# Performance work log

Hardware: AMD Instinct MI355X
Metric: run time of the kernel (lower is better)

The kernel has to match this reference:

```python
import jax, jax.numpy as jnp
import numpy as np
from jax import lax

# BatchNorm2d(affine=False) in eval mode with initial running stats (mean=0, var=1)
# reduces to a constant scale. (Original torch module in train mode would use batch
# stats of the dispatched subset; we use the eval-mode form for a deterministic,
# vectorizable reference.)
BN_SCALE = 1.0 / np.sqrt(1.0 + 1e-5)
DN = ('NCHW', 'OIHW', 'NCHW')


def _dw(x, w, pad, dil=1):
    # depthwise conv, kernel [C,1,k,k]
    return lax.conv_general_dilated(x, w, (1, 1), [(pad, pad), (pad, pad)],
                                    rhs_dilation=(dil, dil), dimension_numbers=DN,
                                    feature_group_count=x.shape[1])


def _pw(x, w):
    # pointwise 1x1 conv, kernel [C,C,1,1]
    return lax.conv_general_dilated(x, w, (1, 1), 'VALID', dimension_numbers=DN)


def _sep(x, d1, p1, d2, p2, pad):
    # DARTS SepConv: (ReLU-dw-pw-BN) x 2
    y = _pw(_dw(jax.nn.relu(x), d1, pad), p1) * BN_SCALE
    return _pw(_dw(jax.nn.relu(y), d2, pad), p2) * BN_SCALE


def _dil(x, d, p, pad):
    # DARTS DilConv: ReLU-dw(dilation=2)-pw-BN
    return _pw(_dw(jax.nn.relu(x), d, pad, 2), p) * BN_SCALE


def _maxpool3(x):
    y = jnp.pad(x, ((0, 0), (0, 0), (1, 1), (1, 1)), constant_values=-jnp.inf)
    return lax.reduce_window(y, -jnp.inf, lax.max, (1, 1, 3, 3), (1, 1, 1, 1), 'VALID')


def _avgpool3(x):
    # avg_pool 3x3 stride 1 pad 1, count_include_pad=False
    pad = [(0, 0), (0, 0), (1, 1), (1, 1)]
    s = lax.reduce_window(x, 0.0, lax.add, (1, 1, 3, 3), (1, 1, 1, 1), pad)
    c = lax.reduce_window(jnp.ones_like(x), 0.0, lax.add, (1, 1, 3, 3), (1, 1, 1, 1), pad)
    return s / c


def _mixed_forward(x, weights, params, top):
    B, n_op = weights.shape
    _, idx = lax.top_k(weights, top)                    # [B, top]
    sel = jax.nn.one_hot(idx, n_op).sum(axis=1) > 0     # [B, n_op] bool: op in top-k
    # softmax over logits masked to -inf outside top-k => non-selected ops weight 0
    gate = jax.nn.softmax(jnp.where(sel, weights, -jnp.inf), axis=-1)  # [B, n_op]
    (sc3_d1, sc3_p1, sc3_d2, sc3_p2,
     sc5_d1, sc5_p1, sc5_d2, sc5_p2,
     dc3_d, dc3_p, dc5_d, dc5_p) = params
    # PRIMITIVES order: none, max_pool_3x3, avg_pool_3x3, skip_connect,
    # sep_conv_3x3, sep_conv_5x5, dil_conv_3x3, dil_conv_5x5
    op_outs = [
        None,                        # 'none' contributes zeros
        _maxpool3(x) * BN_SCALE,     # pool ops are followed by BN(affine=False)
        _avgpool3(x) * BN_SCALE,
        x,                           # skip_connect (stride=1 -> Identity)
        _sep(x, sc3_d1, sc3_p1, sc3_d2, sc3_p2, 1),
        _sep(x, sc5_d1, sc5_p1, sc5_d2, sc5_p2, 2),
        _dil(x, dc3_d, dc3_p, 2),
        _dil(x, dc5_d, dc5_p, 4),
    ]
    out = jnp.zeros_like(x)
    for i, y in enumerate(op_outs):
        if y is not None:
            out = out + gate[:, i, None, None, None] * y
    return out, weights  # second output is gate_value_cp (clone of gate input)


def setup_inputs():
    key = jax.random.key(0)
    ks = jax.random.split(key, 16)
    B, C, H, W = 64, 128, 32, 32
    def p(k, shape):
        return jax.random.normal(k, shape, jnp.float32) * 0.05
    return {
        'x': jax.random.normal(ks[0], (B, C, H, W), jnp.float32),
        'weights': jax.random.normal(ks[1], (B, 8), jnp.float32),
        'sc3_d1': p(ks[2], (C, 1, 3, 3)), 'sc3_p1': p(ks[3], (C, C, 1, 1)),
        'sc3_d2': p(ks[4], (C, 1, 3, 3)), 'sc3_p2': p(ks[5], (C, C, 1, 1)),
        'sc5_d1': p(ks[6], (C, 1, 5, 5)), 'sc5_p1': p(ks[7], (C, C, 1, 1)),
        'sc5_d2': p(ks[8], (C, 1, 5, 5)), 'sc5_p2': p(ks[9], (C, C, 1, 1)),
        'dc3_d': p(ks[10], (C, 1, 3, 3)), 'dc3_p': p(ks[11], (C, C, 1, 1)),
        'dc5_d': p(ks[12], (C, 1, 5, 5)), 'dc5_p': p(ks[13], (C, C, 1, 1)),
        'top': 2,
    }


def reference(x, weights, sc3_d1, sc3_p1, sc3_d2, sc3_p2, sc5_d1, sc5_p1, sc5_d2, sc5_p2, dc3_d, dc3_p, dc5_d, dc5_p, top):
    params = (sc3_d1, sc3_p1, sc3_d2, sc3_p2, sc5_d1, sc5_p1, sc5_d2, sc5_p2,
              dc3_d, dc3_p, dc5_d, dc5_p)
    return _mixed_forward(x, weights, params, top)
```

## Files before the change

kernel.cpp:

```cpp
#include <hip/hip_runtime.h>
#include <hip/hip_bf16.h>


#define BN_SCALE 0.9999950000374997f
#define BB 64
#define CC 128
#define HH 32
#define WW 32
#define PLANE (HH*WW)
#define SAMP (CC*PLANE)
#define NOUT0 (BB*SAMP)

__device__ __forceinline__ float us2f(unsigned int u) {
    unsigned int x = (u & 0xffffu) << 16;
    float f; __builtin_memcpy(&f, &x, 4); return f;
}
__device__ __forceinline__ unsigned short f2us(float f) {
    __hip_bfloat16 h = __float2bfloat16(f);
    unsigned short u; __builtin_memcpy(&u, &h, 2); return u;
}

__global__ void k_gates(const float* __restrict__ wlog,
                        const void* __restrict__ topp,
                        float* __restrict__ gates,
                        int* __restrict__ cnum, int* __restrict__ cops,
                        float* __restrict__ out_w) {
    int b = threadIdx.x;

    int top = -1;
    {
        unsigned int u0 = *(const unsigned int*)topp;
        int i32 = (int)u0;
        if (i32 >= 1 && i32 <= 8) top = i32;
        else {
            float f32; __builtin_memcpy(&f32, &u0, 4);
            if (f32 >= 1.f && f32 <= 8.f) top = (int)(f32 + 0.5f);
            else { float fb = us2f(u0); if (fb >= 1.f && fb <= 8.f) top = (int)(fb + 0.5f); }
        }
        if (top < 1 || top > 8) top = 2;
    }

    float lw[8];
    #pragma unroll
    for (int i = 0; i < 8; ++i) {
        lw[i] = wlog[b * 8 + i];
        out_w[b * 8 + i] = lw[i];
    }
    bool sel[8] = {false,false,false,false,false,false,false,false};
    for (int t = 0; t < top; ++t) {
        int best = -1; float bv = -3.4e38f;
        #pragma unroll
        for (int i = 0; i < 8; ++i)
            if (!sel[i] && lw[i] > bv) { bv = lw[i]; best = i; }
        if (best >= 0) sel[best] = true;
    }
    float m = -3.4e38f;
    #pragma unroll
    for (int i = 0; i < 8; ++i) if (sel[i] && lw[i] > m) m = lw[i];
    float s = 0.f, e[8];
    #pragma unroll
    for (int i = 0; i < 8; ++i) { e[i] = sel[i] ? expf(lw[i] - m) : 0.f; s += e[i]; }
    float inv = (s > 0.f) ? 1.f / s : 0.f;
    float g[8];
    #pragma unroll
    for (int i = 0; i < 8; ++i) {
        g[i] = (s > 0.f) ? e[i] * inv : (sel[i] ? 1.f / (float)top : 0.f);
        gates[b * 8 + i] = g[i];
    }
    int n = 0;
    #pragma unroll
    for (int i = 4; i < 8; ++i)
        if (g[i] > 0.f) { cops[b * 2 + (n < 2 ? n : 1)] = i; ++n; }
    cnum[b] = (n < 2) ? n : 2;
}

template <int K, int DIL>
__device__ __forceinline__ void dw_comp(const float* __restrict__ sx,
                                        const float* __restrict__ wd, int c,
                                        unsigned short* __restrict__ opp) {
    constexpr int PAD = (K / 2) * DIL;
    float wk[K * K];
    #pragma unroll
    for (int i = 0; i < K * K; ++i) wk[i] = wd[c * K * K + i];
    #pragma unroll
    for (int j = 0; j < 4; ++j) {
        int px = threadIdx.x + j * 256;
        int h = px >> 5, w = px & 31;
        float acc = 0.f;
        #pragma unroll
        for (int ky = 0; ky < K; ++ky) {
            int ih = h + ky * DIL - PAD;
            if ((unsigned)ih >= HH) continue;
            #pragma unroll
            for (int kx = 0; kx < K; ++kx) {
                int iw = w + kx * DIL - PAD;
                if ((unsigned)iw >= WW) continue;
                acc = fmaf(wk[ky * K + kx], sx[ih * WW + iw], acc);
            }
        }
        opp[px] = f2us(acc);
    }
}

__global__ __launch_bounds__(256) void
k_dw_first(const float* __restrict__ x,
           const float* __restrict__ w4, const float* __restrict__ w5,
           const float* __restrict__ w6, const float* __restrict__ w7,
           const float* __restrict__ gates,
           unsigned short* __restrict__ A4, unsigned short* __restrict__ A5,
           unsigned short* __restrict__ P6, unsigned short* __restrict__ P7) {
    int plane = blockIdx.x;
    int b = plane >> 7, c = plane & 127;
    float g4 = gates[b * 8 + 4], g5 = gates[b * 8 + 5];
    float g6 = gates[b * 8 + 6], g7 = gates[b * 8 + 7];
    if (g4 == 0.f && g5 == 0.f && g6 == 0.f && g7 == 0.f) return;
    __shared__ float sx[PLANE];
    {
        float4 v = ((const float4*)(x + (size_t)plane * PLANE))[threadIdx.x];
        ((float4*)sx)[threadIdx.x] =
            make_float4(fmaxf(v.x, 0.f), fmaxf(v.y, 0.f),
                        fmaxf(v.z, 0.f), fmaxf(v.w, 0.f));
    }
    __syncthreads();
    size_t off = (size_t)plane * PLANE;
    if (g4 != 0.f) dw_comp<3, 1>(sx, w4, c, A4 + off);
    if (g5 != 0.f) dw_comp<5, 1>(sx, w5, c, A5 + off);
    if (g6 != 0.f) dw_comp<3, 2>(sx, w6, c, P6 + off);
    if (g7 != 0.f) dw_comp<5, 2>(sx, w7, c, P7 + off);
}

__global__ __launch_bounds__(256) void
k_dw_second(const unsigned short* __restrict__ B4,
            const unsigned short* __restrict__ B5,
            const float* __restrict__ w4, const float* __restrict__ w5,
            const float* __restrict__ gates,
            unsigned short* __restrict__ P4, unsigned short* __restrict__ P5) {
    int plane = blockIdx.x;
    int b = plane >> 7, c = plane & 127;
    float g4 = gates[b * 8 + 4], g5 = gates[b * 8 + 5];
    if (g4 == 0.f && g5 == 0.f) return;
    __shared__ float sx[PLANE];
    size_t off = (size_t)plane * PLANE;
    if (g4 != 0.f) {
        ushort4 v = ((const ushort4*)(B4 + off))[threadIdx.x];
        ((float4*)sx)[threadIdx.x] =
            make_float4(fmaxf(us2f(v.x), 0.f), fmaxf(us2f(v.y), 0.f),
                        fmaxf(us2f(v.z), 0.f), fmaxf(us2f(v.w), 0.f));
        __syncthreads();
        dw_comp<3, 1>(sx, w4, c, P4 + off);
        __syncthreads();
    }
    if (g5 != 0.f) {
        ushort4 v = ((const ushort4*)(B5 + off))[threadIdx.x];
        ((float4*)sx)[threadIdx.x] =
            make_float4(fmaxf(us2f(v.x), 0.f), fmaxf(us2f(v.y), 0.f),
                        fmaxf(us2f(v.z), 0.f), fmaxf(us2f(v.w), 0.f));
        __syncthreads();
        dw_comp<5, 1>(sx, w5, c, P5 + off);
    }
}

__device__ __forceinline__ void pw_acc(const unsigned short* __restrict__ ib,
                                       const float* __restrict__ W,
                                       int co0, int hw, float2* acc) {
    for (int ci = 0; ci < CC; ++ci) {
        unsigned int raw = *reinterpret_cast<const unsigned int*>(ib + ci * PLANE + hw);
        float vx = us2f(raw), vy = us2f(raw >> 16);
        #pragma unroll
        for (int k = 0; k < 8; ++k) {
            float wv = W[(co0 + k) * CC + ci];
            acc[k].x = fmaf(wv, vx, acc[k].x);
            acc[k].y = fmaf(wv, vy, acc[k].y);
        }
    }
}

__global__ __launch_bounds__(256) void
k_pw_mid(const unsigned short* __restrict__ A4,
         const unsigned short* __restrict__ A5,
         const float* __restrict__ W4, const float* __restrict__ W5,
         const float* __restrict__ gates,
         unsigned short* __restrict__ B4, unsigned short* __restrict__ B5) {
    int blk = blockIdx.x;
    int hws = blk & 1;
    int cog = (blk >> 1) & 15;
    int b   = (blk >> 5) & 63;
    int opi = blk >> 11;
    float g = gates[b * 8 + 4 + opi];
    if (g == 0.f) return;
    const unsigned short* in = (opi ? A5 : A4) + (size_t)b * SAMP;
    const float* W = opi ? W5 : W4;
    unsigned short* ob = (opi ? B5 : B4);
    int co0 = cog * 8;
    int hw = hws * 512 + threadIdx.x * 2;
    float2 acc[8];
    #pragma unroll
    for (int k = 0; k < 8; ++k) acc[k] = make_float2(0.f, 0.f);
    pw_acc(in, W, co0, hw, acc);
    #pragma unroll
    for (int k = 0; k < 8; ++k) {
        size_t idx = (size_t)(b * CC + co0 + k) * PLANE + hw;
        unsigned int* p = reinterpret_cast<unsigned int*>(ob + idx);
        *p = (unsigned int)f2us(BN_SCALE * acc[k].x) |
             ((unsigned int)f2us(BN_SCALE * acc[k].y) << 16);
    }
}

__global__ __launch_bounds__(256) void
k_pw_final(const float* __restrict__ x,
           const unsigned short* __restrict__ P4,
           const unsigned short* __restrict__ P5,
           const unsigned short* __restrict__ P6,
           const unsigned short* __restrict__ P7,
           const float* __restrict__ W4, const float* __restrict__ W5,
           const float* __restrict__ W6, const float* __restrict__ W7,
           const float* __restrict__ gates,
           const int* __restrict__ cnum, const int* __restrict__ cops,
           float* __restrict__ out) {
    int blk = blockIdx.x;
    int hws = blk & 1;
    int cog = (blk >> 1) & 15;
    int b = blk >> 5;
    int co0 = cog * 8;
    int hw = hws * 512 + threadIdx.x * 2;

    float g1 = gates[b * 8 + 1] * BN_SCALE;
    float g2 = gates[b * 8 + 2] * BN_SCALE;
    float g3 = gates[b * 8 + 3];
    bool haspool = (g1 != 0.f) | (g2 != 0.f) | (g3 != 0.f);

    __shared__ float sxp[8 * 18 * 32];
    int r0 = hws * 16;
    if (haspool) {
        for (int li = threadIdx.x; li < 8 * 18 * 8; li += 256) {
            int ch = li / 144, rem = li - ch * 144;
            int row = rem >> 3, c4 = rem & 7;
            int gr = r0 + row - 1;
            if ((unsigned)gr < HH) {
                float4 v = *(const float4*)(x + ((size_t)(b * CC + co0 + ch) * HH + gr) * WW + c4 * 4);
                *(float4*)(sxp + (ch * 18 + row) * 32 + c4 * 4) = v;
            }
        }
        __syncthreads();
    }

    float2 acc[8];
    #pragma unroll
    for (int k = 0; k < 8; ++k) acc[k] = make_float2(0.f, 0.f);
    int n = cnum[b];
    for (int t = 0; t < n; ++t) {
        int op = cops[b * 2 + t];
        float gs = gates[b * 8 + op] * BN_SCALE;
        const unsigned short* src;
        const float* W;
        switch (op) {
            case 4:  src = P4; W = W4; break;
            case 5:  src = P5; W = W5; break;
            case 6:  src = P6; W = W6; break;
            default: src = P7; W = W7; break;
        }
        float2 a2[8];
        #pragma unroll
        for (int k = 0; k < 8; ++k) a2[k] = make_float2(0.f, 0.f);
        pw_acc(src + (size_t)b * SAMP, W, co0, hw, a2);
        #pragma unroll
        for (int k = 0; k < 8; ++k) {
            acc[k].x = fmaf(gs, a2[k].x, acc[k].x);
            acc[k].y = fmaf(gs, a2[k].y, acc[k].y);
        }
    }

    int h = hw >> 5, w = hw & 31;
    int lr = h - r0 + 1;
    #pragma unroll
    for (int k = 0; k < 8; ++k) {
        float2 o = acc[k];
        if (haspool) {
            const float* sp = sxp + k * 18 * 32;
            #pragma unroll
            for (int jj = 0; jj < 2; ++jj) {
                int ww = w + jj;
                float mx = -3.4e38f, sm = 0.f;
                int cnt = 0;
                #pragma unroll
                for (int dh = -1; dh <= 1; ++dh) {
                    int ih = h + dh;
                    if ((unsigned)ih >= HH) continue;
                    #pragma unroll
                    for (int dw = -1; dw <= 1; ++dw) {
                        int iw = ww + dw;
                        if ((unsigned)iw >= WW) continue;
                        float v = sp[(lr + dh) * 32 + iw];
                        mx = fmaxf(mx, v);
                        sm += v;
                        ++cnt;
                    }
                }
                float pv = g1 * mx + g2 * (sm / (float)cnt) + g3 * sp[lr * 32 + ww];
                if (jj == 0) o.x += pv; else o.y += pv;
            }
        }
        *(float2*)(out + (size_t)(b * CC + co0 + k) * PLANE + hw) = o;
    }
}

extern "C" void kernel_launch(void* const* d_in, const int* in_sizes, int n_in,
                              void* d_out, int out_size, void* d_ws, size_t ws_size,
                              hipStream_t stream) {
    const float* x      = (const float*)d_in[0];
    const float* wlog   = (const float*)d_in[1];
    const float* sc3_d1 = (const float*)d_in[2];
    const float* sc3_p1 = (const float*)d_in[3];
    const float* sc3_d2 = (const float*)d_in[4];
    const float* sc3_p2 = (const float*)d_in[5];
    const float* sc5_d1 = (const float*)d_in[6];
    const float* sc5_p1 = (const float*)d_in[7];
    const float* sc5_d2 = (const float*)d_in[8];
    const float* sc5_p2 = (const float*)d_in[9];
    const float* dc3_d  = (const float*)d_in[10];
    const float* dc3_p  = (const float*)d_in[11];
    const float* dc5_d  = (const float*)d_in[12];
    const float* dc5_p  = (const float*)d_in[13];
    const void* topp    = d_in[14];

    float* out  = (float*)d_out;
    float* outw = out + NOUT0;

    float* gates = (float*)d_ws;
    int*   cnum  = (int*)((char*)d_ws + 2048);
    int*   cops  = (int*)((char*)d_ws + 2304);
    unsigned short* base = (unsigned short*)((char*)d_ws + 4096);
    unsigned short* A4 = base;
    unsigned short* A5 = base + (size_t)NOUT0;
    unsigned short* B4 = base + (size_t)NOUT0 * 2;
    unsigned short* B5 = base + (size_t)NOUT0 * 3;
    unsigned short* P4 = base + (size_t)NOUT0 * 4;
    unsigned short* P5 = base + (size_t)NOUT0 * 5;
    unsigned short* P6 = base + (size_t)NOUT0 * 6;
    unsigned short* P7 = base + (size_t)NOUT0 * 7;

    k_gates<<<1, 64, 0, stream>>>(wlog, topp, gates, cnum, cops, outw);
    k_dw_first<<<BB * CC, 256, 0, stream>>>(x, sc3_d1, sc5_d1, dc3_d, dc5_d,
                                            gates, A4, A5, P6, P7);
    k_pw_mid<<<2 * BB * 32, 256, 0, stream>>>(A4, A5, sc3_p1, sc5_p1, gates, B4, B5);
    k_dw_second<<<BB * CC, 256, 0, stream>>>(B4, B5, sc3_d2, sc5_d2, gates, P4, P5);
    k_pw_final<<<BB * 32, 256, 0, stream>>>(x, P4, P5, P6, P7,
                                            sc3_p2, sc5_p2, dc3_p, dc5_p,
                                            gates, cnum, cops, out);
}
```

Baseline: 209.4 us.

## Stage pointwise weights in LDS and widen per-thread register tiles

The pointwise conv kernels now stage a 16-output-channel weight slice in shared memory, padded to avoid bank conflicts and pre-scaled by BN scale or gate. Each thread computes 8 channels by 4 pixels instead of 8 by 2, halving the grid and doubling reuse of each activation load. The pool input tile is stored in shared memory as bf16, which halves LDS use but rounds the pool inputs. The cops buffer grows to 4 entries per sample, and the extra block syncs add overhead for each selected op.

```diff
diff --git a/kernel.cpp b/kernel.cpp
--- a/kernel.cpp
+++ b/kernel.cpp
@@ -70,8 +70,8 @@
     int n = 0;
     #pragma unroll
     for (int i = 4; i < 8; ++i)
-        if (g[i] > 0.f) { cops[b * 2 + (n < 2 ? n : 1)] = i; ++n; }
-    cnum[b] = (n < 2) ? n : 2;
+        if (g[i] > 0.f) { if (n < 4) cops[b * 4 + n] = i; ++n; }
+    cnum[b] = (n < 4) ? n : 4;
 }
 
 template <int K, int DIL>
@@ -160,17 +160,35 @@
     }
 }
 
-__device__ __forceinline__ void pw_acc(const unsigned short* __restrict__ ib,
-                                       const float* __restrict__ W,
-                                       int co0, int hw, float2* acc) {
+#define WLROW 17
+
+__device__ __forceinline__ void stage_w(float* __restrict__ Wl,
+                                        const float* __restrict__ W,
+                                        int co0, float s) {
+    #pragma unroll
+    for (int i = 0; i < 8; ++i) {
+        int idx = threadIdx.x + i * 256;
+        int c = idx >> 7, ci = idx & 127;
+        Wl[ci * WLROW + c] = W[(co0 + c) * CC + ci] * s;
+    }
+}
+
+__device__ __forceinline__ void pw_fat(const unsigned short* __restrict__ ib,
+                                       const float* __restrict__ Wl,
+                                       int cg, int hw, float acc[8][4]) {
+    const float* wr0 = Wl + cg * 8;
     for (int ci = 0; ci < CC; ++ci) {
-        unsigned int raw = *reinterpret_cast<const unsigned int*>(ib + ci * PLANE + hw);
-        float vx = us2f(raw), vy = us2f(raw >> 16);
+        uint2 raw = *reinterpret_cast<const uint2*>(ib + ci * PLANE + hw);
+        float v0 = us2f(raw.x), v1 = us2f(raw.x >> 16);
+        float v2 = us2f(raw.y), v3 = us2f(raw.y >> 16);
+        const float* wr = wr0 + ci * WLROW;
         #pragma unroll
         for (int k = 0; k < 8; ++k) {
-            float wv = W[(co0 + k) * CC + ci];
-            acc[k].x = fmaf(wv, vx, acc[k].x);
-            acc[k].y = fmaf(wv, vy, acc[k].y);
+            float wv = wr[k];
+            acc[k][0] = fmaf(wv, v0, acc[k][0]);
+            acc[k][1] = fmaf(wv, v1, acc[k][1]);
+            acc[k][2] = fmaf(wv, v2, acc[k][2]);
+            acc[k][3] = fmaf(wv, v3, acc[k][3]);
         }
     }
 }
@@ -182,27 +200,28 @@
          const float* __restrict__ gates,
          unsigned short* __restrict__ B4, unsigned short* __restrict__ B5) {
     int blk = blockIdx.x;
-    int hws = blk & 1;
-    int cog = (blk >> 1) & 15;
-    int b   = (blk >> 5) & 63;
-    int opi = blk >> 11;
-    float g = gates[b * 8 + 4 + opi];
-    if (g == 0.f) return;
-    const unsigned short* in = (opi ? A5 : A4) + (size_t)b * SAMP;
-    const float* W = opi ? W5 : W4;
-    unsigned short* ob = (opi ? B5 : B4);
-    int co0 = cog * 8;
-    int hw = hws * 512 + threadIdx.x * 2;
-    float2 acc[8];
-    #pragma unroll
-    for (int k = 0; k < 8; ++k) acc[k] = make_float2(0.f, 0.f);
-    pw_acc(in, W, co0, hw, acc);
+    int tile = blk & 15;
+    int opi  = (blk >> 4) & 1;
+    int b    = blk >> 5;
+    if (gates[b * 8 + 4 + opi] == 0.f) return;
+    int cog = tile >> 1, hws = tile & 1;
+    int co0 = cog * 16;
+    int cg = threadIdx.x >> 7, ht = threadIdx.x & 127;
+    int hw = hws * 512 + ht * 4;
+    __shared__ float Wl[128 * WLROW];
+    stage_w(Wl, opi ? W5 : W4, co0, BN_SCALE);
+    __syncthreads();
+    const unsigned short* ib = (opi ? A5 : A4) + (size_t)b * SAMP;
+    float acc[8][4] = {};
+    pw_fat(ib, Wl, cg, hw, acc);
+    unsigned short* ob = opi ? B5 : B4;
     #pragma unroll
     for (int k = 0; k < 8; ++k) {
-        size_t idx = (size_t)(b * CC + co0 + k) * PLANE + hw;
-        unsigned int* p = reinterpret_cast<unsigned int*>(ob + idx);
-        *p = (unsigned int)f2us(BN_SCALE * acc[k].x) |
-             ((unsigned int)f2us(BN_SCALE * acc[k].y) << 16);
+        size_t idx = (size_t)(b * CC + co0 + cg * 8 + k) * PLANE + hw;
+        uint2 pk;
+        pk.x = (unsigned int)f2us(acc[k][0]) | ((unsigned int)f2us(acc[k][1]) << 16);
+        pk.y = (unsigned int)f2us(acc[k][2]) | ((unsigned int)f2us(acc[k][3]) << 16);
+        *reinterpret_cast<uint2*>(ob + idx) = pk;
     }
 }
 
@@ -218,38 +237,41 @@
            const int* __restrict__ cnum, const int* __restrict__ cops,
            float* __restrict__ out) {
     int blk = blockIdx.x;
-    int hws = blk & 1;
-    int cog = (blk >> 1) & 15;
-    int b = blk >> 5;
-    int co0 = cog * 8;
-    int hw = hws * 512 + threadIdx.x * 2;
+    int tile = blk & 15;
+    int b    = blk >> 4;
+    int cog = tile >> 1, hws = tile & 1;
+    int co0 = cog * 16;
+    int cg = threadIdx.x >> 7, ht = threadIdx.x & 127;
+    int hw = hws * 512 + ht * 4;
 
     float g1 = gates[b * 8 + 1] * BN_SCALE;
     float g2 = gates[b * 8 + 2] * BN_SCALE;
     float g3 = gates[b * 8 + 3];
     bool haspool = (g1 != 0.f) | (g2 != 0.f) | (g3 != 0.f);
 
-    __shared__ float sxp[8 * 18 * 32];
+    __shared__ float Wl[128 * WLROW];
+    __shared__ unsigned short sxp[16 * 18 * 32];
+
     int r0 = hws * 16;
     if (haspool) {
-        for (int li = threadIdx.x; li < 8 * 18 * 8; li += 256) {
+        for (int li = threadIdx.x; li < 16 * 18 * 8; li += 256) {
             int ch = li / 144, rem = li - ch * 144;
             int row = rem >> 3, c4 = rem & 7;
             int gr = r0 + row - 1;
             if ((unsigned)gr < HH) {
                 float4 v = *(const float4*)(x + ((size_t)(b * CC + co0 + ch) * HH + gr) * WW + c4 * 4);
-                *(float4*)(sxp + (ch * 18 + row) * 32 + c4 * 4) = v;
+                ushort4 pv;
+                pv.x = f2us(v.x); pv.y = f2us(v.y); pv.z = f2us(v.z); pv.w = f2us(v.w);
+                *(ushort4*)(sxp + (ch * 18 + row) * 32 + c4 * 4) = pv;
             }
         }
-        __syncthreads();
-    }
-
-    float2 acc[8];
-    #pragma unroll
-    for (int k = 0; k < 8; ++k) acc[k] = make_float2(0.f, 0.f);
+    }
+    __syncthreads();
+
+    float acc[8][4] = {};
     int n = cnum[b];
     for (int t = 0; t < n; ++t) {
-        int op = cops[b * 2 + t];
+        int op = cops[b * 4 + t];
         float gs = gates[b * 8 + op] * BN_SCALE;
         const unsigned short* src;
         const float* W;
@@ -259,26 +281,20 @@
             case 6:  src = P6; W = W6; break;
             default: src = P7; W = W7; break;
         }
-        float2 a2[8];
-        #pragma unroll
-        for (int k = 0; k < 8; ++k) a2[k] = make_float2(0.f, 0.f);
-        pw_acc(src + (size_t)b * SAMP, W, co0, hw, a2);
-        #pragma unroll
-        for (int k = 0; k < 8; ++k) {
-            acc[k].x = fmaf(gs, a2[k].x, acc[k].x);
-            acc[k].y = fmaf(gs, a2[k].y, acc[k].y);
-        }
+        __syncthreads();
+        stage_w(Wl, W, co0, gs);
+        __syncthreads();
+        pw_fat(src + (size_t)b * SAMP, Wl, cg, hw, acc);
     }
 
     int h = hw >> 5, w = hw & 31;
     int lr = h - r0 + 1;
     #pragma unroll
     for (int k = 0; k < 8; ++k) {
-        float2 o = acc[k];
         if (haspool) {
-            const float* sp = sxp + k * 18 * 32;
+            const unsigned short* sp = sxp + (cg * 8 + k) * 18 * 32;
             #pragma unroll
-            for (int jj = 0; jj < 2; ++jj) {
+            for (int jj = 0; jj < 4; ++jj) {
                 int ww = w + jj;
                 float mx = -3.4e38f, sm = 0.f;
                 int cnt = 0;
@@ -290,17 +306,18 @@
                     for (int dw = -1; dw <= 1; ++dw) {
                         int iw = ww + dw;
                         if ((unsigned)iw >= WW) continue;
-                        float v = sp[(lr + dh) * 32 + iw];
+                        float v = us2f(sp[(lr + dh) * 32 + iw]);
                         mx = fmaxf(mx, v);
                         sm += v;
                         ++cnt;
                     }
                 }
-                float pv = g1 * mx + g2 * (sm / (float)cnt) + g3 * sp[lr * 32 + ww];
-                if (jj == 0) o.x += pv; else o.y += pv;
+                acc[k][jj] += g1 * mx + g2 * (sm / (float)cnt)
+                            + g3 * us2f(sp[lr * 32 + ww]);
             }
         }
-        *(float2*)(out + (size_t)(b * CC + co0 + k) * PLANE + hw) = o;
+        *(float4*)(out + (size_t)(b * CC + co0 + cg * 8 + k) * PLANE + hw) =
+            make_float4(acc[k][0], acc[k][1], acc[k][2], acc[k][3]);
     }
 }
 
@@ -342,9 +359,9 @@
     k_gates<<<1, 64, 0, stream>>>(wlog, topp, gates, cnum, cops, outw);
     k_dw_first<<<BB * CC, 256, 0, stream>>>(x, sc3_d1, sc5_d1, dc3_d, dc5_d,
                                             gates, A4, A5, P6, P7);
-    k_pw_mid<<<2 * BB * 32, 256, 0, stream>>>(A4, A5, sc3_p1, sc5_p1, gates, B4, B5);
+    k_pw_mid<<<BB * 32, 256, 0, stream>>>(A4, A5, sc3_p1, sc5_p1, gates, B4, B5);
     k_dw_second<<<BB * CC, 256, 0, stream>>>(B4, B5, sc3_d2, sc5_d2, gates, P4, P5);
-    k_pw_final<<<BB * 32, 256, 0, stream>>>(x, P4, P5, P6, P7,
+    k_pw_final<<<BB * 16, 256, 0, stream>>>(x, P4, P5, P6, P7,
                                             sc3_p2, sc5_p2, dc3_p, dc5_p,
                                             gates, cnum, cops, out);
 }
```

New measurement: 214.2 us. +2.3%, slower.

## Use bf16 MFMA for pointwise convs and split pooling into separate kernel

Applied to the files above, without the earlier changes.

Replaces the scalar FMA pointwise 1x1 convolutions in the mid and final stages with LDS-staged bf16 MFMA 16x16x32 tiles. Each block computes 64 output channels by 64 pixels, with weights converted to bf16 and the gate scale folded in. Pooling and skip terms move to a new per-plane kernel that writes the output first, and the final pointwise kernel then accumulates into it with a read-modify-write. The weights are now rounded to bf16, which adds precision error, and the extra pass plus output reread adds memory traffic.

```diff
diff --git a/kernel.cpp b/kernel.cpp
--- a/kernel.cpp
+++ b/kernel.cpp
@@ -10,6 +10,10 @@
 #define PLANE (HH*WW)
 #define SAMP (CC*PLANE)
 #define NOUT0 (BB*SAMP)
+#define LROW 136
+
+typedef __attribute__((ext_vector_type(8))) short bf16x8;
+typedef __attribute__((ext_vector_type(4))) float f32x4;
 
 __device__ __forceinline__ float us2f(unsigned int u) {
     unsigned int x = (u & 0xffffu) << 16;
@@ -70,8 +74,49 @@
     int n = 0;
     #pragma unroll
     for (int i = 4; i < 8; ++i)
-        if (g[i] > 0.f) { cops[b * 2 + (n < 2 ? n : 1)] = i; ++n; }
-    cnum[b] = (n < 2) ? n : 2;
+        if (g[i] > 0.f) { if (n < 4) cops[b * 4 + n] = i; ++n; }
+    cnum[b] = (n < 4) ? n : 4;
+}
+
+__global__ __launch_bounds__(256) void
+k_pools(const float* __restrict__ x,
+        const float* __restrict__ gates,
+        float* __restrict__ out) {
+    int plane = blockIdx.x;
+    int b = plane >> 7;
+    float g1 = gates[b * 8 + 1] * BN_SCALE;
+    float g2 = gates[b * 8 + 2] * BN_SCALE;
+    float g3 = gates[b * 8 + 3];
+    float* op = out + (size_t)plane * PLANE;
+    if (g1 == 0.f && g2 == 0.f && g3 == 0.f) {
+        ((float4*)op)[threadIdx.x] = make_float4(0.f, 0.f, 0.f, 0.f);
+        return;
+    }
+    __shared__ float sx[PLANE];
+    ((float4*)sx)[threadIdx.x] = ((const float4*)(x + (size_t)plane * PLANE))[threadIdx.x];
+    __syncthreads();
+    #pragma unroll
+    for (int j = 0; j < 4; ++j) {
+        int px = threadIdx.x + j * 256;
+        int h = px >> 5, w = px & 31;
+        float mx = -3.4e38f, sm = 0.f;
+        int cnt = 0;
+        #pragma unroll
+        for (int dh = -1; dh <= 1; ++dh) {
+            int ih = h + dh;
+            if ((unsigned)ih >= HH) continue;
+            #pragma unroll
+            for (int dw = -1; dw <= 1; ++dw) {
+                int iw = w + dw;
+                if ((unsigned)iw >= WW) continue;
+                float v = sx[ih * WW + iw];
+                mx = fmaxf(mx, v);
+                sm += v;
+                ++cnt;
+            }
+        }
+        op[px] = g1 * mx + g2 * (sm / (float)cnt) + g3 * sx[px];
+    }
 }
 
 template <int K, int DIL>
@@ -160,17 +205,46 @@
     }
 }
 
-__device__ __forceinline__ void pw_acc(const unsigned short* __restrict__ ib,
-                                       const float* __restrict__ W,
-                                       int co0, int hw, float2* acc) {
-    for (int ci = 0; ci < CC; ++ci) {
-        unsigned int raw = *reinterpret_cast<const unsigned int*>(ib + ci * PLANE + hw);
-        float vx = us2f(raw), vy = us2f(raw >> 16);
-        #pragma unroll
-        for (int k = 0; k < 8; ++k) {
-            float wv = W[(co0 + k) * CC + ci];
-            acc[k].x = fmaf(wv, vx, acc[k].x);
-            acc[k].y = fmaf(wv, vy, acc[k].y);
+
+__device__ __forceinline__ void stage_wt(unsigned short* __restrict__ Wt,
+                                         const float* __restrict__ W,
+                                         int co0, float s) {
+    unsigned int* Wtu = (unsigned int*)Wt;
+    #pragma unroll
+    for (int i = 0; i < 16; ++i) {
+        int idx = threadIdx.x + i * 256;
+        int r = idx >> 6, c2 = idx & 63;
+        float2 v = *(const float2*)(W + (size_t)(co0 + r) * CC + c2 * 2);
+        Wtu[r * (LROW / 2) + c2] =
+            (unsigned int)f2us(v.x * s) | ((unsigned int)f2us(v.y * s) << 16);
+    }
+}
+
+__device__ __forceinline__ void stage_bt(unsigned short* __restrict__ Bt,
+                                         const unsigned short* __restrict__ ib,
+                                         int hw0) {
+    #pragma unroll
+    for (int i = 0; i < 16; ++i) {
+        int idx = threadIdx.x + i * 256;
+        int ci = idx >> 5, hp = (idx & 31) * 2;
+        unsigned int raw = *(const unsigned int*)(ib + (size_t)ci * PLANE + hw0 + hp);
+        Bt[hp * LROW + ci]       = (unsigned short)(raw & 0xffffu);
+        Bt[(hp + 1) * LROW + ci] = (unsigned short)(raw >> 16);
+    }
+}
+
+__device__ __forceinline__ void mfma_tile(const unsigned short* __restrict__ Wt,
+                                          const unsigned short* __restrict__ Bt,
+                                          int wave, int quad, int m,
+                                          f32x4 acc[4]) {
+    #pragma unroll
+    for (int kb = 0; kb < 4; ++kb) {
+        int cio = kb * 32 + quad * 8;
+        bf16x8 a = *(const bf16x8*)(Wt + (wave * 16 + m) * LROW + cio);
+        #pragma unroll
+        for (int nt = 0; nt < 4; ++nt) {
+            bf16x8 bv = *(const bf16x8*)(Bt + (nt * 16 + m) * LROW + cio);
+            acc[nt] = __builtin_amdgcn_mfma_f32_16x16x32_bf16(a, bv, acc[nt], 0, 0, 0);
         }
     }
 }
@@ -182,33 +256,43 @@
          const float* __restrict__ gates,
          unsigned short* __restrict__ B4, unsigned short* __restrict__ B5) {
     int blk = blockIdx.x;
-    int hws = blk & 1;
-    int cog = (blk >> 1) & 15;
-    int b   = (blk >> 5) & 63;
-    int opi = blk >> 11;
-    float g = gates[b * 8 + 4 + opi];
-    if (g == 0.f) return;
-    const unsigned short* in = (opi ? A5 : A4) + (size_t)b * SAMP;
-    const float* W = opi ? W5 : W4;
-    unsigned short* ob = (opi ? B5 : B4);
-    int co0 = cog * 8;
-    int hw = hws * 512 + threadIdx.x * 2;
-    float2 acc[8];
-    #pragma unroll
-    for (int k = 0; k < 8; ++k) acc[k] = make_float2(0.f, 0.f);
-    pw_acc(in, W, co0, hw, acc);
-    #pragma unroll
-    for (int k = 0; k < 8; ++k) {
-        size_t idx = (size_t)(b * CC + co0 + k) * PLANE + hw;
-        unsigned int* p = reinterpret_cast<unsigned int*>(ob + idx);
-        *p = (unsigned int)f2us(BN_SCALE * acc[k].x) |
-             ((unsigned int)f2us(BN_SCALE * acc[k].y) << 16);
-    }
-}
-
-__global__ __launch_bounds__(256) void
-k_pw_final(const float* __restrict__ x,
-           const unsigned short* __restrict__ P4,
+    int hwt = blk & 15;
+    int coh = (blk >> 4) & 1;
+    int b = blk >> 5;
+    float g4 = gates[b * 8 + 4], g5 = gates[b * 8 + 5];
+    if (g4 == 0.f && g5 == 0.f) return;
+    int co0 = coh * 64, hw0 = hwt * 64;
+    int wave = threadIdx.x >> 6, lane = threadIdx.x & 63;
+    int quad = lane >> 4, m = lane & 15;
+    __shared__ unsigned short Wt[64 * LROW];
+    __shared__ unsigned short Bt[64 * LROW];
+    bool staged = false;
+    #pragma unroll
+    for (int opi = 0; opi < 2; ++opi) {
+        if ((opi ? g5 : g4) == 0.f) continue;
+        if (staged) __syncthreads();
+        stage_wt(Wt, opi ? W5 : W4, co0, BN_SCALE);
+        stage_bt(Bt, (opi ? A5 : A4) + (size_t)b * SAMP, hw0);
+        __syncthreads();
+        f32x4 acc[4];
+        #pragma unroll
+        for (int i = 0; i < 4; ++i) acc[i] = (f32x4){0.f, 0.f, 0.f, 0.f};
+        mfma_tile(Wt, Bt, wave, quad, m, acc);
+        unsigned short* ob = opi ? B5 : B4;
+        #pragma unroll
+        for (int nt = 0; nt < 4; ++nt)
+            #pragma unroll
+            for (int r = 0; r < 4; ++r) {
+                int co = co0 + wave * 16 + quad * 4 + r;
+                int col = hw0 + nt * 16 + m;
+                ob[(size_t)(b * CC + co) * PLANE + col] = f2us(acc[nt][r]);
+            }
+        staged = true;
+    }
+}
+
+__global__ __launch_bounds__(256) void
+k_pw_final(const unsigned short* __restrict__ P4,
            const unsigned short* __restrict__ P5,
            const unsigned short* __restrict__ P6,
            const unsigned short* __restrict__ P7,
@@ -218,38 +302,21 @@
            const int* __restrict__ cnum, const int* __restrict__ cops,
            float* __restrict__ out) {
     int blk = blockIdx.x;
-    int hws = blk & 1;
-    int cog = (blk >> 1) & 15;
+    int hwt = blk & 15;
+    int coh = (blk >> 4) & 1;
     int b = blk >> 5;
-    int co0 = cog * 8;
-    int hw = hws * 512 + threadIdx.x * 2;
-
-    float g1 = gates[b * 8 + 1] * BN_SCALE;
-    float g2 = gates[b * 8 + 2] * BN_SCALE;
-    float g3 = gates[b * 8 + 3];
-    bool haspool = (g1 != 0.f) | (g2 != 0.f) | (g3 != 0.f);
-
-    __shared__ float sxp[8 * 18 * 32];
-    int r0 = hws * 16;
-    if (haspool) {
-        for (int li = threadIdx.x; li < 8 * 18 * 8; li += 256) {
-            int ch = li / 144, rem = li - ch * 144;
-            int row = rem >> 3, c4 = rem & 7;
-            int gr = r0 + row - 1;
-            if ((unsigned)gr < HH) {
-                float4 v = *(const float4*)(x + ((size_t)(b * CC + co0 + ch) * HH + gr) * WW + c4 * 4);
-                *(float4*)(sxp + (ch * 18 + row) * 32 + c4 * 4) = v;
-            }
-        }
-        __syncthreads();
-    }
-
-    float2 acc[8];
-    #pragma unroll
-    for (int k = 0; k < 8; ++k) acc[k] = make_float2(0.f, 0.f);
     int n = cnum[b];
+    if (n == 0) return;
+    int co0 = coh * 64, hw0 = hwt * 64;
+    int wave = threadIdx.x >> 6, lane = threadIdx.x & 63;
+    int quad = lane >> 4, m = lane & 15;
+    __shared__ unsigned short Wt[64 * LROW];
+    __shared__ unsigned short Bt[64 * LROW];
+    f32x4 acc[4];
+    #pragma unroll
+    for (int i = 0; i < 4; ++i) acc[i] = (f32x4){0.f, 0.f, 0.f, 0.f};
     for (int t = 0; t < n; ++t) {
-        int op = cops[b * 2 + t];
+        int op = cops[b * 4 + t];
         float gs = gates[b * 8 + op] * BN_SCALE;
         const unsigned short* src;
         const float* W;
@@ -259,49 +326,21 @@
             case 6:  src = P6; W = W6; break;
             default: src = P7; W = W7; break;
         }
-        float2 a2[8];
-        #pragma unroll
-        for (int k = 0; k < 8; ++k) a2[k] = make_float2(0.f, 0.f);
-        pw_acc(src + (size_t)b * SAMP, W, co0, hw, a2);
-        #pragma unroll
-        for (int k = 0; k < 8; ++k) {
-            acc[k].x = fmaf(gs, a2[k].x, acc[k].x);
-            acc[k].y = fmaf(gs, a2[k].y, acc[k].y);
-        }
-    }
-
-    int h = hw >> 5, w = hw & 31;
-    int lr = h - r0 + 1;
-    #pragma unroll
-    for (int k = 0; k < 8; ++k) {
-        float2 o = acc[k];
-        if (haspool) {
-            const float* sp = sxp + k * 18 * 32;
-            #pragma unroll
-            for (int jj = 0; jj < 2; ++jj) {
-                int ww = w + jj;
-                float mx = -3.4e38f, sm = 0.f;
-                int cnt = 0;
-                #pragma unroll
-                for (int dh = -1; dh <= 1; ++dh) {
-                    int ih = h + dh;
-                    if ((unsigned)ih >= HH) continue;
-                    #pragma unroll
-                    for (int dw = -1; dw <= 1; ++dw) {
-                        int iw = ww + dw;
-                        if ((unsigned)iw >= WW) continue;
-                        float v = sp[(lr + dh) * 32 + iw];
-                        mx = fmaxf(mx, v);
-                        sm += v;
-                        ++cnt;
-                    }
-                }
-                float pv = g1 * mx + g2 * (sm / (float)cnt) + g3 * sp[lr * 32 + ww];
-                if (jj == 0) o.x += pv; else o.y += pv;
-            }
-        }
-        *(float2*)(out + (size_t)(b * CC + co0 + k) * PLANE + hw) = o;
-    }
+        if (t) __syncthreads();
+        stage_wt(Wt, W, co0, gs);
+        stage_bt(Bt, src + (size_t)b * SAMP, hw0);
+        __syncthreads();
+        mfma_tile(Wt, Bt, wave, quad, m, acc);
+    }
+    #pragma unroll
+    for (int nt = 0; nt < 4; ++nt)
+        #pragma unroll
+        for (int r = 0; r < 4; ++r) {
+            int co = co0 + wave * 16 + quad * 4 + r;
+            int col = hw0 + nt * 16 + m;
+            size_t idx = (size_t)(b * CC + co) * PLANE + col;
+            out[idx] += acc[nt][r];
+        }
 }
 
 extern "C" void kernel_launch(void* const* d_in, const int* in_sizes, int n_in,
@@ -340,11 +379,12 @@
     unsigned short* P7 = base + (size_t)NOUT0 * 7;
 
     k_gates<<<1, 64, 0, stream>>>(wlog, topp, gates, cnum, cops, outw);
+    k_pools<<<BB * CC, 256, 0, stream>>>(x, gates, out);
     k_dw_first<<<BB * CC, 256, 0, stream>>>(x, sc3_d1, sc5_d1, dc3_d, dc5_d,
                                             gates, A4, A5, P6, P7);
-    k_pw_mid<<<2 * BB * 32, 256, 0, stream>>>(A4, A5, sc3_p1, sc5_p1, gates, B4, B5);
+    k_pw_mid<<<BB * 32, 256, 0, stream>>>(A4, A5, sc3_p1, sc5_p1, gates, B4, B5);
     k_dw_second<<<BB * CC, 256, 0, stream>>>(B4, B5, sc3_d2, sc5_d2, gates, P4, P5);
-    k_pw_final<<<BB * 32, 256, 0, stream>>>(x, P4, P5, P6, P7,
+    k_pw_final<<<BB * 32, 256, 0, stream>>>(P4, P5, P6, P7,
                                             sc3_p2, sc5_p2, dc3_p, dc5_p,
                                             gates, cnum, cops, out);
 }
```

New measurement: 196.9 us. 1.06x faster.
